# Performance work log

Hardware: AMD Instinct MI355X
Metric: run time of the kernel (lower is better)

## Reference

```python
import jax, jax.numpy as jnp
import numpy as np

R = 16
LORA_ALPHA = 16
SCALING = LORA_ALPHA / R  # 1.0


def setup_inputs() -> dict:
    key = jax.random.key(0)
    kx, kr, ka = jax.random.split(key, 3)
    B, S, D, DO, E = 4, 2048, 4096, 4096, 8
    x = jax.random.normal(kx, (B, S, D), dtype=jnp.float32)
    # kaiming_uniform_(a=sqrt(5)) on Linear weight of fan_in=D -> U(-1/sqrt(D), 1/sqrt(D))
    bound_r = 1.0 / np.sqrt(D)
    route_w = jax.random.uniform(kr, (E, D), jnp.float32, -bound_r, bound_r)  # lora_route.weight
    bound_a = 1.0 / np.sqrt(D)
    A = jax.random.uniform(ka, (E, R, D), jnp.float32, -bound_a, bound_a)  # stacked lora_A{i}.weight [r, D]
    # lora_B weights are zero-initialized in the module; use small random for a nontrivial baseline
    kb = jax.random.fold_in(key, 7)
    Bw = jax.random.normal(kb, (E, DO, R), dtype=jnp.float32) * 0.02  # stacked lora_B{i}.weight [DO, r]
    return {"x": x, "route_w": route_w, "A": A, "Bw": Bw}


def reference(x, route_w, A, Bw):
    # router logits [B, S, E]
    logits = jnp.einsum("bsd,ed->bse", x, route_w)
    # top-1 hard routing: keep raw logit value at the argmax slot, zero elsewhere
    topk_v, topk_idx = jax.lax.top_k(logits, 1)  # [B,S,1]
    E = logits.shape[-1]
    route_weight = jax.nn.one_hot(topk_idx[..., 0], E, dtype=logits.dtype) * topk_v  # [B,S,E]
    # low-rank per-expert projections (dense over experts, as in the original loop)
    h = jnp.einsum("bsd,erd->bser", x, A)            # [B,S,E,r]
    wh = route_weight[..., None] * h                  # weight before the up-projection
    out = jnp.einsum("bser,eor->bso", wh, Bw) * SCALING  # [B,S,DO]
    return out
```

## Files before the change

kernel.cpp:

```cpp
#include <hip/hip_runtime.h>
#include <hip/hip_bf16.h>

#define DD   4096
#define NE   8
#define NR   16
#define NTOK 8192
#define NDO  4096

typedef __attribute__((ext_vector_type(8))) __bf16 bf16x8;
typedef __attribute__((ext_vector_type(4))) float  f32x4;

__device__ __forceinline__ bf16x8 to_bf16x8(float4 a, float4 b) {
    bf16x8 r;
    r[0] = (__bf16)a.x; r[1] = (__bf16)a.y; r[2] = (__bf16)a.z; r[3] = (__bf16)a.w;
    r[4] = (__bf16)b.x; r[5] = (__bf16)b.y; r[6] = (__bf16)b.z; r[7] = (__bf16)b.w;
    return r;
}

__global__ __launch_bounds__(64) void k_zero(int* __restrict__ count) {
    if (threadIdx.x < NE) count[threadIdx.x] = 0;
}

__global__ __launch_bounds__(256) void k_route(const float* __restrict__ x,
                                               const float* __restrict__ rw,
                                               float* __restrict__ w_arr,
                                               int*   __restrict__ token_list,
                                               int*   __restrict__ count) {
    const int wave = threadIdx.x >> 6;
    const int lane = threadIdx.x & 63;
    const int t0   = blockIdx.x * 16 + wave * 4;
    const float* xp = x + (size_t)t0 * DD;

    __shared__ float rws[NE][1024];

    double acc[4][NE];
    #pragma unroll
    for (int t = 0; t < 4; t++)
        #pragma unroll
        for (int e = 0; e < NE; e++) acc[t][e] = 0.0;

    for (int c = 0; c < 4; c++) {
        __syncthreads();
        #pragma unroll
        for (int i = 0; i < 8; i++) {
            const int j  = i * 256 + threadIdx.x;
            const int e  = j >> 8;
            const int d4 = (j & 255) * 4;
            *(float4*)&rws[e][d4] =
                *(const float4*)(rw + (size_t)e * DD + c * 1024 + d4);
        }
        __syncthreads();

        #pragma unroll
        for (int i = 0; i < 4; i++) {
            const int dc = (i * 64 + lane) * 4;
            double xd[4][4];
            #pragma unroll
            for (int t = 0; t < 4; t++) {
                const float4 xv = *(const float4*)(xp + (size_t)t * DD + c * 1024 + dc);
                xd[t][0] = xv.x; xd[t][1] = xv.y; xd[t][2] = xv.z; xd[t][3] = xv.w;
            }
            #pragma unroll
            for (int e = 0; e < NE; e++) {
                const float4 wv = *(const float4*)&rws[e][dc];
                const double w0 = wv.x, w1 = wv.y, w2 = wv.z, w3 = wv.w;
                #pragma unroll
                for (int t = 0; t < 4; t++) {
                    acc[t][e] = fma(xd[t][0], w0, acc[t][e]);
                    acc[t][e] = fma(xd[t][1], w1, acc[t][e]);
                    acc[t][e] = fma(xd[t][2], w2, acc[t][e]);
                    acc[t][e] = fma(xd[t][3], w3, acc[t][e]);
                }
            }
        }
    }

    #pragma unroll
    for (int off = 32; off > 0; off >>= 1) {
        #pragma unroll
        for (int t = 0; t < 4; t++)
            #pragma unroll
            for (int e = 0; e < NE; e++)
                acc[t][e] += __shfl_xor(acc[t][e], off, 64);
    }

    #pragma unroll
    for (int tt = 0; tt < 4; tt++) {
        if (lane == tt) {
            double best = acc[tt][0]; int be = 0;
            #pragma unroll
            for (int e = 1; e < NE; e++)
                if (acc[tt][e] > best) { best = acc[tt][e]; be = e; }
            const int tok = t0 + tt;
            w_arr[tok] = (float)best;
            const int pos = atomicAdd(&count[be], 1);
            token_list[be * NTOK + pos] = tok;
        }
    }
}

__global__ __launch_bounds__(512) void k_h(const float* __restrict__ x,
                                           const float* __restrict__ Am,
                                           const float* __restrict__ w_arr,
                                           const int*   __restrict__ token_list,
                                           const int*   __restrict__ count,
                                           __hip_bfloat16* __restrict__ wh) {
    const int e    = blockIdx.x >> 9;
    const int g    = blockIdx.x & 511;
    const int cnt  = count[e];
    const int base = g * 16;
    if (base >= cnt) return;

    const int wv   = threadIdx.x >> 6;
    const int lane = threadIdx.x & 63;
    const int m    = lane & 15;
    const int half = lane >> 4;

    const int  idx   = base + m;
    const bool valid = idx < cnt;
    const int  tok   = valid ? token_list[e * NTOK + idx] : 0;
    const float* xrow = x  + (size_t)tok * DD;
    const float* arow = Am + ((size_t)e * NR + m) * DD;

    f32x4 acc = {0.f, 0.f, 0.f, 0.f};
    const int kbase = wv * 512;
    #pragma unroll 4
    for (int ks = 0; ks < 16; ks++) {
        const int k0 = kbase + ks * 32 + half * 8;
        const float4 xa = *(const float4*)(xrow + k0);
        const float4 xb = *(const float4*)(xrow + k0 + 4);
        const float4 aa = *(const float4*)(arow + k0);
        const float4 ab = *(const float4*)(arow + k0 + 4);
        const bf16x8 af = to_bf16x8(xa, xb);
        const bf16x8 bf = to_bf16x8(aa, ab);
        acc = __builtin_amdgcn_mfma_f32_16x16x32_bf16(af, bf, acc, 0, 0, 0);
    }

    __shared__ float lds[8][16][20];
    #pragma unroll
    for (int r = 0; r < 4; r++) lds[wv][half * 4 + r][m] = acc[r];
    __syncthreads();

    if (threadIdx.x < 256) {
        const int t = threadIdx.x >> 4;
        const int r = threadIdx.x & 15;
        const int i2 = base + t;
        if (i2 < cnt) {
            float s = 0.f;
            #pragma unroll
            for (int w = 0; w < 8; w++) s += lds[w][t][r];
            const int tk = token_list[e * NTOK + i2];
            wh[(size_t)tk * NR + r] = (__hip_bfloat16)(s * w_arr[tk]);
        }
    }
}

__global__ __launch_bounds__(256) void k_out(const float* __restrict__ Bw,
                                             const __hip_bfloat16* __restrict__ wh,
                                             const int*   __restrict__ token_list,
                                             const int*   __restrict__ count,
                                             float* __restrict__ out) {
    const int bx    = blockIdx.x;
    const int chunk = bx & 3;
    const int slot  = (bx >> 2) & 511;
    const int e     = bx >> 11;
    const int cnt   = count[e];
    const int base  = slot * 16;
    if (base >= cnt) return;

    const int wv   = threadIdx.x >> 6;
    const int lane = threadIdx.x & 63;
    const int m    = lane & 15;
    const int half = lane >> 4;

    const int  idx   = base + m;
    const bool valid = idx < cnt;
    const int  tok   = valid ? token_list[e * NTOK + idx] : 0;

    bf16x8 a2;
    if (half < 2 && valid) {
        a2 = *(const bf16x8*)(wh + (size_t)tok * NR + half * 8);
    } else {
        #pragma unroll
        for (int j = 0; j < 8; j++) a2[j] = (__bf16)0.0f;
    }

    int trow[4]; bool vrow[4];
    #pragma unroll
    for (int r = 0; r < 4; r++) {
        const int ir = base + half * 4 + r;
        vrow[r] = ir < cnt;
        trow[r] = vrow[r] ? token_list[e * NTOK + ir] : 0;
    }

    const float* bwe = Bw + (size_t)e * NDO * NR;
    const int h2 = (half < 2) ? half : 0;
    const f32x4 zero4 = {0.f, 0.f, 0.f, 0.f};
    const int ob0 = chunk * 1024 + wv * 256;

    #pragma unroll 4
    for (int ot = 0; ot < 16; ot++) {
        const int obase = ob0 + ot * 16;
        const float* bp = bwe + (size_t)(obase + m) * NR + h2 * 8;
        const float4 p = *(const float4*)(bp);
        const float4 q = *(const float4*)(bp + 4);
        bf16x8 b2 = to_bf16x8(p, q);
        if (half >= 2) {
            #pragma unroll
            for (int j = 0; j < 8; j++) b2[j] = (__bf16)0.0f;
        }
        const f32x4 d = __builtin_amdgcn_mfma_f32_16x16x32_bf16(a2, b2, zero4, 0, 0, 0);
        #pragma unroll
        for (int r = 0; r < 4; r++) {
            if (vrow[r]) out[(size_t)trow[r] * NDO + obase + m] = d[r];
        }
    }
}

extern "C" void kernel_launch(void* const* d_in, const int* in_sizes, int n_in,
                              void* d_out, int out_size, void* d_ws, size_t ws_size,
                              hipStream_t stream) {
    const float* x  = (const float*)d_in[0];
    const float* rw = (const float*)d_in[1];
    const float* Am = (const float*)d_in[2];
    const float* Bw = (const float*)d_in[3];
    float* out = (float*)d_out;

    char* ws = (char*)d_ws;
    int*   count      = (int*)ws;
    float* w_arr      = (float*)(ws + 512);
    int*   token_list = (int*)(ws + 65536);
    __hip_bfloat16* wh = (__hip_bfloat16*)(ws + 65536 + NE * NTOK * 4);

    hipLaunchKernelGGL(k_zero,  dim3(1),     dim3(64),  0, stream, count);
    hipLaunchKernelGGL(k_route, dim3(512),   dim3(256), 0, stream, x, rw, w_arr, token_list, count);
    hipLaunchKernelGGL(k_h,     dim3(4096),  dim3(512), 0, stream, x, Am, w_arr, token_list, count, wh);
    hipLaunchKernelGGL(k_out,   dim3(16384), dim3(256), 0, stream, Bw, wh, token_list, count, out);
}
```

Measured before the change: 180.6 us.

## Split router dot product across waves and drop LDS staging of router weights

The router kernel now gives each block 4 tokens, with each of its 4 waves covering a quarter of the hidden dimension, so it launches 2048 blocks instead of 512. Router weights are read straight from global memory (likely cache-resident) instead of being staged through LDS, and the per-wave partial sums are combined in shared memory before the argmax. The aim is more parallelism and fewer block-wide barriers in the FP64 router pass. The separate zeroing kernel is replaced by hipMemsetAsync. The cost is an extra cross-wave reduction and more repeated global reads of the router weights.

```diff
diff --git a/kernel.cpp b/kernel.cpp
--- a/kernel.cpp
+++ b/kernel.cpp
@@ -17,21 +17,16 @@
     return r;
 }
 
-__global__ __launch_bounds__(64) void k_zero(int* __restrict__ count) {
-    if (threadIdx.x < NE) count[threadIdx.x] = 0;
-}
-
 __global__ __launch_bounds__(256) void k_route(const float* __restrict__ x,
                                                const float* __restrict__ rw,
                                                float* __restrict__ w_arr,
                                                int*   __restrict__ token_list,
                                                int*   __restrict__ count) {
-    const int wave = threadIdx.x >> 6;
+    const int wv   = threadIdx.x >> 6;
     const int lane = threadIdx.x & 63;
-    const int t0   = blockIdx.x * 16 + wave * 4;
+    const int t0   = blockIdx.x * 4;
     const float* xp = x + (size_t)t0 * DD;
-
-    __shared__ float rws[NE][1024];
+    const int dbase = wv * 1024;
 
     double acc[4][NE];
     #pragma unroll
@@ -39,38 +34,25 @@
         #pragma unroll
         for (int e = 0; e < NE; e++) acc[t][e] = 0.0;
 
-    for (int c = 0; c < 4; c++) {
-        __syncthreads();
-        #pragma unroll
-        for (int i = 0; i < 8; i++) {
-            const int j  = i * 256 + threadIdx.x;
-            const int e  = j >> 8;
-            const int d4 = (j & 255) * 4;
-            *(float4*)&rws[e][d4] =
-                *(const float4*)(rw + (size_t)e * DD + c * 1024 + d4);
-        }
-        __syncthreads();
-
-        #pragma unroll
-        for (int i = 0; i < 4; i++) {
-            const int dc = (i * 64 + lane) * 4;
-            double xd[4][4];
+    #pragma unroll
+    for (int i = 0; i < 4; i++) {
+        const int d4 = dbase + (i * 64 + lane) * 4;
+        double xd[4][4];
+        #pragma unroll
+        for (int t = 0; t < 4; t++) {
+            const float4 xv = *(const float4*)(xp + (size_t)t * DD + d4);
+            xd[t][0] = xv.x; xd[t][1] = xv.y; xd[t][2] = xv.z; xd[t][3] = xv.w;
+        }
+        #pragma unroll
+        for (int e = 0; e < NE; e++) {
+            const float4 wv4 = *(const float4*)(rw + (size_t)e * DD + d4);
+            const double w0 = wv4.x, w1 = wv4.y, w2 = wv4.z, w3 = wv4.w;
             #pragma unroll
             for (int t = 0; t < 4; t++) {
-                const float4 xv = *(const float4*)(xp + (size_t)t * DD + c * 1024 + dc);
-                xd[t][0] = xv.x; xd[t][1] = xv.y; xd[t][2] = xv.z; xd[t][3] = xv.w;
-            }
-            #pragma unroll
-            for (int e = 0; e < NE; e++) {
-                const float4 wv = *(const float4*)&rws[e][dc];
-                const double w0 = wv.x, w1 = wv.y, w2 = wv.z, w3 = wv.w;
-                #pragma unroll
-                for (int t = 0; t < 4; t++) {
-                    acc[t][e] = fma(xd[t][0], w0, acc[t][e]);
-                    acc[t][e] = fma(xd[t][1], w1, acc[t][e]);
-                    acc[t][e] = fma(xd[t][2], w2, acc[t][e]);
-                    acc[t][e] = fma(xd[t][3], w3, acc[t][e]);
-                }
+                acc[t][e] = fma(xd[t][0], w0, acc[t][e]);
+                acc[t][e] = fma(xd[t][1], w1, acc[t][e]);
+                acc[t][e] = fma(xd[t][2], w2, acc[t][e]);
+                acc[t][e] = fma(xd[t][3], w3, acc[t][e]);
             }
         }
     }
@@ -84,18 +66,24 @@
                 acc[t][e] += __shfl_xor(acc[t][e], off, 64);
     }
 
-    #pragma unroll
-    for (int tt = 0; tt < 4; tt++) {
-        if (lane == tt) {
-            double best = acc[tt][0]; int be = 0;
-            #pragma unroll
-            for (int e = 1; e < NE; e++)
-                if (acc[tt][e] > best) { best = acc[tt][e]; be = e; }
-            const int tok = t0 + tt;
-            w_arr[tok] = (float)best;
-            const int pos = atomicAdd(&count[be], 1);
-            token_list[be * NTOK + pos] = tok;
-        }
+    __shared__ double red[4][4][NE];
+    if (lane < 32) red[wv][lane >> 3][lane & 7] = acc[lane >> 3][lane & 7];
+    __syncthreads();
+    if (threadIdx.x < 32) {
+        const int t = threadIdx.x >> 3, e = threadIdx.x & 7;
+        red[0][t][e] = red[0][t][e] + red[1][t][e] + red[2][t][e] + red[3][t][e];
+    }
+    __syncthreads();
+    if (threadIdx.x < 4) {
+        const int t = threadIdx.x;
+        double best = red[0][t][0]; int be = 0;
+        #pragma unroll
+        for (int e = 1; e < NE; e++)
+            if (red[0][t][e] > best) { best = red[0][t][e]; be = e; }
+        const int tok = t0 + t;
+        w_arr[tok] = (float)best;
+        const int pos = atomicAdd(&count[be], 1);
+        token_list[be * NTOK + pos] = tok;
     }
 }
 
@@ -232,8 +220,8 @@
     int*   token_list = (int*)(ws + 65536);
     __hip_bfloat16* wh = (__hip_bfloat16*)(ws + 65536 + NE * NTOK * 4);
 
-    hipLaunchKernelGGL(k_zero,  dim3(1),     dim3(64),  0, stream, count);
-    hipLaunchKernelGGL(k_route, dim3(512),   dim3(256), 0, stream, x, rw, w_arr, token_list, count);
+    hipMemsetAsync(count, 0, NE * sizeof(int), stream);
+    hipLaunchKernelGGL(k_route, dim3(2048),  dim3(256), 0, stream, x, rw, w_arr, token_list, count);
     hipLaunchKernelGGL(k_h,     dim3(4096),  dim3(512), 0, stream, x, Am, w_arr, token_list, count, wh);
     hipLaunchKernelGGL(k_out,   dim3(16384), dim3(256), 0, stream, Bw, wh, token_list, count, out);
 }
```

Result: slower. 201.9 us (+11.8%).
